# Kernel tuning notes

Hardware: AMD Instinct MI355X
Metric: run time of the kernel (lower is better)

Reference implementation:

```python
import jax, jax.numpy as jnp
import numpy as np

N, E, C, S = 30000, 480000, 256, 4
T_EVO = 0.1        # evolution_time
MAX_EIG = 0.5      # max_eigenval in create_ultra_stable_hamiltonian
MAX_NORM = 0.01    # max_norm in ultra_stable_matrix_exp
MAX_TERMS = 4
LN_EPS = 1e-5


def _build_subgraphs(edge_index, n, s):
    """Emulates the per-node k_hop=1 BFS (capped at max_subgraph_size=s) and the
    subgraph laplacian Hamiltonian build (edge_weight=0.1, self-loops added).
    Pure structural preprocessing: integer/constant w.r.t. all float params."""
    src = np.asarray(edge_index[0], dtype=np.int64)
    dst = np.asarray(edge_index[1], dtype=np.int64)
    loops = np.arange(n, dtype=np.int64)
    src = np.concatenate([src, loops]); dst = np.concatenate([dst, loops])
    order = np.argsort(src, kind='stable')
    src_s, dst_s = src[order], dst[order]
    starts = np.searchsorted(src_s, np.arange(n))
    ends = np.searchsorted(src_s, np.arange(n) + 1)
    edge_set = set((src * n + dst).tolist())
    sub_nodes = np.zeros((n, s), dtype=np.int64)
    sub_mask = np.zeros((n, s), dtype=np.float32)
    H = np.zeros((n, s, s), dtype=np.float32)
    for i in range(n):
        nbrs = [i]
        for d in dst_s[starts[i]:ends[i]]:
            d = int(d)
            if d != i and d not in nbrs:
                nbrs.append(d)
                if len(nbrs) == s:
                    break
        m = len(nbrs)
        sub_nodes[i, :m] = nbrs
        sub_nodes[i, m:] = i          # pad with center (masked out below)
        sub_mask[i, :m] = 1.0
        A = np.zeros((s, s), dtype=np.float32)
        for a in range(m):
            ka = nbrs[a] * n
            for b in range(m):
                if (ka + nbrs[b]) in edge_set:
                    A[a, b] = 1.0
        deg = np.maximum(A.sum(axis=1), 1e-6)   # degree(row), clamped like torch
        H[i] = np.diag(deg) - 0.1 * A           # laplacian with edge_weight=0.1
    return sub_nodes, sub_mask, H


def _mat_fro(M):
    return jnp.sqrt(jnp.sum(jnp.abs(M) ** 2, axis=(-2, -1)))


def _unitary_from_H(sub_H):
    """ultra_stable_matrix_exp, batched over N tiny [S,S] Hamiltonians.
    The torch .item() norm/eigenvalue rescales detach gradients, so treating this
    whole block as parameter-independent (it is: H is structural) is faithful."""
    Hc = sub_H.astype(jnp.complex64)
    ev = jnp.linalg.eigvals(Hc)                              # [N,S] (CPU op)
    mx = jnp.max(ev.real, axis=-1)
    Hc = Hc * jnp.where(mx > MAX_EIG, MAX_EIG / mx, 1.0)[:, None, None]
    hn = _mat_fro(Hc)
    Hc = Hc * jnp.where(hn > MAX_NORM, MAX_NORM / hn, 1.0)[:, None, None]
    A = (-1j) * Hc * (T_EVO * 0.1)                           # scaled_H
    I = jnp.eye(S, dtype=jnp.complex64)
    U = jnp.broadcast_to(I, Hc.shape)
    term = U
    for k in range(1, MAX_TERMS + 1):
        term = jnp.matmul(term, A) / k
        tn = _mat_fro(term)
        term = term * jnp.where(tn > 0.1, 0.1 / tn, 1.0)[:, None, None]
        U = U + term
    err = _mat_fro(jnp.matmul(U, jnp.conj(jnp.swapaxes(U, -1, -2))) - I)
    U = jnp.where((err > 0.1)[:, None, None], I + A * 0.01, U)
    return U


def _cplx_linear(xr, xi, wr, wi, br, bi):
    xr = jnp.clip(xr, -10.0, 10.0); xi = jnp.clip(xi, -10.0, 10.0)
    re = xr @ wr.T - xi @ wi.T + br
    im = xr @ wi.T + xi @ wr.T + bi
    return re + 1j * im


def _cln(z, w, b, eps=LN_EPS):
    # UltraStableComplexLayerNorm, training-mode batch stats over dim 0
    mag = jnp.clip(jnp.sqrt(z.real ** 2 + z.imag ** 2 + eps), eps, 1000.0)
    mean = mag.mean(0)
    var = mag.var(0)
    nm = (mag - mean) / (jnp.sqrt(var + eps) + eps)
    sm = jnp.clip(nm * jnp.abs(w) + b, eps, 10.0)
    ph = jnp.arctan2(jnp.clip(z.imag, -1e6, 1e6), jnp.clip(z.real, -1e6, 1e6) + 1e-10)
    return sm * jnp.cos(ph) + 1j * (sm * jnp.sin(ph))


def _crelu(z, leak=0.01, mx=5.0):
    r = jnp.clip(z.real, -mx, mx); i = jnp.clip(z.imag, -mx, mx)
    return jnp.where(r > 0, r, leak * r) + 1j * jnp.where(i > 0, i, leak * i)


def setup_inputs() -> dict:
    key = jax.random.key(0)
    k1, k2, k3, k4 = jax.random.split(key, 4)
    x = jax.random.normal(k1, (N, C), dtype=jnp.float32)
    edge_index = jax.random.randint(k2, (2, E), 0, N, dtype=jnp.int64)
    sub_nodes, sub_mask, sub_H = _build_subgraphs(np.asarray(edge_index), N, S)
    std = np.sqrt(0.5 / C).astype(np.float32)
    w_real = jax.random.normal(k3, (C, C), dtype=jnp.float32) * std
    w_imag = jax.random.normal(k4, (C, C), dtype=jnp.float32) * std
    return {
        'x': x,
        'edge_index': edge_index,
        'sub_nodes': jnp.asarray(sub_nodes),
        'sub_mask': jnp.asarray(sub_mask),
        'sub_H': jnp.asarray(sub_H),
        'w_real': w_real,
        'w_imag': w_imag,
        'b_real': jnp.zeros((C,), jnp.float32),
        'b_imag': jnp.zeros((C,), jnp.float32),
        'ln_weight': jnp.full((C,), 0.1, jnp.float32),
        'ln_bias': jnp.zeros((C,), jnp.float32),
        'evolution_scale': jnp.asarray(0.1, jnp.float32),
    }


def reference(x, edge_index, sub_nodes, sub_mask, sub_H,
              w_real, w_imag, b_real, b_imag, ln_weight, ln_bias,
              evolution_scale):
    # complex linear (input is real -> imag part zero, matching torch.complex(x, 0*x))
    h = _cplx_linear(x, jnp.zeros_like(x), w_real, w_imag, b_real, b_imag)  # [N,C] c64
    U = _unitary_from_H(sub_H)                                              # [N,S,S]
    sub_x = h[sub_nodes] * sub_mask[..., None]                              # [N,S,C]
    # center node is slot 0 of each subgraph -> take row 0 of U @ sub_x
    evolved = jnp.einsum('ns,nsc->nc', U[:, 0, :], sub_x)
    out = evolved * evolution_scale + x.astype(jnp.complex64)  # residual (in==out)
    out = _cln(out, ln_weight, ln_bias)
    out = _crelu(out)
    # dropout is eval-mode identity
    return jnp.concatenate([out.real, out.imag], axis=-1)      # [N, 2C] float32
```

## Files before the change

### kernel.cpp

```cpp
#include <hip/hip_runtime.h>
#include <stdint.h>

#define N_NODES 30000
#define NC 256

typedef _Float16 f16x8 __attribute__((ext_vector_type(8)));
typedef _Float16 f16x4 __attribute__((ext_vector_type(4)));
typedef _Float16 f16x2 __attribute__((ext_vector_type(2)));
typedef float f32x4 __attribute__((ext_vector_type(4)));

__global__ void k_conv_x(const float* __restrict__ x, _Float16* __restrict__ xb) {
    int i = (blockIdx.x * 256 + threadIdx.x) * 4;
    float4 v = *reinterpret_cast<const float4*>(x + i);
    f16x4 o;
    o[0] = (_Float16)fminf(fmaxf(v.x, -10.f), 10.f);
    o[1] = (_Float16)fminf(fmaxf(v.y, -10.f), 10.f);
    o[2] = (_Float16)fminf(fmaxf(v.z, -10.f), 10.f);
    o[3] = (_Float16)fminf(fmaxf(v.w, -10.f), 10.f);
    *reinterpret_cast<f16x4*>(xb + i) = o;
}

__global__ void k_conv_w(const float* __restrict__ wr, const float* __restrict__ wi,
                         _Float16* __restrict__ Wb) {
    int i = (blockIdx.x * 256 + threadIdx.x) * 4;
    const float* src = (i < NC * NC) ? (wr + i) : (wi + (i - NC * NC));
    float4 v = *reinterpret_cast<const float4*>(src);
    f16x4 o;
    o[0] = (_Float16)v.x; o[1] = (_Float16)v.y;
    o[2] = (_Float16)v.z; o[3] = (_Float16)v.w;
    *reinterpret_cast<f16x4*>(Wb + i) = o;
}

__global__ void k_prep(const float* __restrict__ subH, const float* __restrict__ sub_mask,
                       const float* __restrict__ escp, float* __restrict__ c4) {
    int node = blockIdx.x * 256 + threadIdx.x;
    if (node >= N_NODES) return;
    float esc = *escp;
    const float4* Hp = reinterpret_cast<const float4*>(subH + node * 16);
    float4 r0 = Hp[0], r1 = Hp[1], r2 = Hp[2], r3 = Hp[3];
    float fr = r0.x * r0.x + r0.y * r0.y + r0.z * r0.z + r0.w * r0.w
             + r1.x * r1.x + r1.y * r1.y + r1.z * r1.z + r1.w * r1.w
             + r2.x * r2.x + r2.y * r2.y + r2.z * r2.z + r2.w * r2.w
             + r3.x * r3.x + r3.y * r3.y + r3.z * r3.z + r3.w * r3.w;
    float coef = 1e-4f * rsqrtf(fr) * esc;
    float4 m = *reinterpret_cast<const float4*>(sub_mask + node * 4);
    float4 o;
    o.x = coef * r0.x * m.x;
    o.y = coef * r0.y * m.y;
    o.z = coef * r0.z * m.z;
    o.w = coef * r0.w * m.w;
    *reinterpret_cast<float4*>(c4 + node * 4) = o;
}

__global__ __launch_bounds__(256, 2) void k_gemm(
    const _Float16* __restrict__ A, const _Float16* __restrict__ B,
    const float* __restrict__ br, const float* __restrict__ bi,
    _Float16* __restrict__ H)
{
    int bid = blockIdx.x;
    int bm = bid >> 1, cs = bid & 1;
    int tid = threadIdx.x;
    int lane = tid & 63, wave = tid >> 6;
    int quad = lane >> 4, l16 = lane & 15;
    int wm = wave >> 1, wn = wave & 1;
    int row0 = bm * 128 + wm * 64;

    f16x8 af[4][8];
#pragma unroll
    for (int mi = 0; mi < 4; mi++) {
        int r = row0 + mi * 16 + l16;
        if (r >= N_NODES) r = N_NODES - 1;
        const _Float16* ap = A + r * NC + quad * 8;
#pragma unroll
        for (int kc = 0; kc < 8; kc++)
            af[mi][kc] = *reinterpret_cast<const f16x8*>(ap + kc * 32);
    }

    const float* bias_p = wn ? bi : br;
#pragma unroll
    for (int cn = 0; cn < 2; cn++) {
        const _Float16* bbase = B + ((wn ? 256 : 0) + cs * 128 + cn * 64 + l16) * NC
                                  + quad * 8;
        f16x8 bb[2][4];
#pragma unroll
        for (int ni = 0; ni < 4; ni++)
            bb[0][ni] = *reinterpret_cast<const f16x8*>(bbase + ni * 16 * NC);
        f32x4 acc[4][4] = {};
#pragma unroll
        for (int kc = 0; kc < 8; kc++) {
            int cur = kc & 1, nxt = cur ^ 1;
            if (kc < 7) {
#pragma unroll
                for (int ni = 0; ni < 4; ni++)
                    bb[nxt][ni] = *reinterpret_cast<const f16x8*>(
                        bbase + ni * 16 * NC + (kc + 1) * 32);
            }
#pragma unroll
            for (int mi = 0; mi < 4; mi++)
#pragma unroll
                for (int ni = 0; ni < 4; ni++)
                    acc[mi][ni] = __builtin_amdgcn_mfma_f32_16x16x32_f16(
                        af[mi][kc], bb[cur][ni], acc[mi][ni], 0, 0, 0);
        }
#pragma unroll
        for (int ni = 0; ni < 4; ni++) {
            int c = cs * 128 + cn * 64 + ni * 16 + l16;
            float bias = bias_p[c];
            int cc = 2 * c + wn;
#pragma unroll
            for (int mi = 0; mi < 4; mi++) {
                int rowb = row0 + mi * 16 + quad * 4;
#pragma unroll
                for (int r = 0; r < 4; r++) {
                    int row = rowb + r;
                    if (row < N_NODES)
                        H[row * 512 + cc] = (_Float16)(acc[mi][ni][r] + bias);
                }
            }
        }
    }
}

#define NPB 60
#define NGRP 8
__global__ __launch_bounds__(512) void k_evolve(
    const float* __restrict__ x, const int* __restrict__ sub_nodes,
    const float* __restrict__ c4, const _Float16* __restrict__ h,
    const float* __restrict__ escp,
    float* __restrict__ outz, _Float16* __restrict__ zbuf, int use_f16,
    float* __restrict__ ssum, float* __restrict__ ssumsq)
{
    __shared__ int   s_nodes[NPB][4];
    __shared__ float s_P[NPB][4];
    __shared__ float s_redA[NGRP][256];
    __shared__ float s_redB[NGRP][256];
    int tid = threadIdx.x;
    int g = tid >> 6, lane = tid & 63;
    int base = blockIdx.x * NPB;
    if (tid < NPB) {
        int node = base + tid;
        *reinterpret_cast<float4*>(&s_P[tid][0]) =
            *reinterpret_cast<const float4*>(c4 + node * 4);
        *reinterpret_cast<int4*>(&s_nodes[tid][0]) =
            *reinterpret_cast<const int4*>(sub_nodes + node * 4);
    }
    __syncthreads();
    float esc = *escp;
    float lsum[4] = {0.f, 0.f, 0.f, 0.f};
    float lsq[4]  = {0.f, 0.f, 0.f, 0.f};

    f16x8 hvA[4];
    float4 xA;
    int j = g;
#pragma unroll
    for (int s = 0; s < 4; s++)
        hvA[s] = *reinterpret_cast<const f16x8*>(h + s_nodes[j][s] * 512 + lane * 8);
    xA = *reinterpret_cast<const float4*>(x + (base + j) * NC + lane * 4);

    for (;;) {
        int jn = j + NGRP;
        bool more = jn < NPB;
        f16x8 hvB[4];
        float4 xB;
        if (more) {
#pragma unroll
            for (int s = 0; s < 4; s++)
                hvB[s] = *reinterpret_cast<const f16x8*>(
                    h + s_nodes[jn][s] * 512 + lane * 8);
            xB = *reinterpret_cast<const float4*>(x + (base + jn) * NC + lane * 4);
        }
        {
            int node = base + j;
            float P0 = s_P[j][0], P1 = s_P[j][1], P2 = s_P[j][2], P3 = s_P[j][3];
            float xr[4] = {xA.x, xA.y, xA.z, xA.w};
            f16x8 zo;
            float or4[4], oi4[4];
#pragma unroll
            for (int e = 0; e < 4; e++) {
                float hr0 = (float)hvA[0][2 * e], hi0 = (float)hvA[0][2 * e + 1];
                float hr1 = (float)hvA[1][2 * e], hi1 = (float)hvA[1][2 * e + 1];
                float hr2 = (float)hvA[2][2 * e], hi2 = (float)hvA[2][2 * e + 1];
                float hr3 = (float)hvA[3][2 * e], hi3 = (float)hvA[3][2 * e + 1];
                float er = esc * hr0;
                float ei = esc * hi0;
                er = fmaf(P0, hi0, er); ei = fmaf(-P0, hr0, ei);
                er = fmaf(P1, hi1, er); ei = fmaf(-P1, hr1, ei);
                er = fmaf(P2, hi2, er); ei = fmaf(-P2, hr2, ei);
                er = fmaf(P3, hi3, er); ei = fmaf(-P3, hr3, ei);
                float outr = er + xr[e];
                float outi = ei;
                or4[e] = outr; oi4[e] = outi;
                zo[2 * e] = (_Float16)outr; zo[2 * e + 1] = (_Float16)outi;
                float mag = sqrtf(fmaf(outr, outr, fmaf(outi, outi, 1e-5f)));
                mag = fminf(fmaxf(mag, 1e-5f), 1000.f);
                lsum[e] += mag;
                lsq[e] = fmaf(mag, mag, lsq[e]);
            }
            if (use_f16) {
                *reinterpret_cast<f16x8*>(zbuf + node * 512 + lane * 8) = zo;
            } else {
                *reinterpret_cast<float4*>(outz + node * 512 + lane * 4) =
                    make_float4(or4[0], or4[1], or4[2], or4[3]);
                *reinterpret_cast<float4*>(outz + node * 512 + 256 + lane * 4) =
                    make_float4(oi4[0], oi4[1], oi4[2], oi4[3]);
            }
        }
        if (!more) break;
#pragma unroll
        for (int s = 0; s < 4; s++) hvA[s] = hvB[s];
        xA = xB;
        j = jn;
    }
#pragma unroll
    for (int e = 0; e < 4; e++) {
        s_redA[g][lane * 4 + e] = lsum[e];
        s_redB[g][lane * 4 + e] = lsq[e];
    }
    __syncthreads();
    if (tid < 256) {
        float a = 0.f;
#pragma unroll
        for (int q = 0; q < NGRP; q++) a += s_redA[q][tid];
        atomicAdd(&ssum[tid], a);
    } else {
        int t = tid - 256;
        float b = 0.f;
#pragma unroll
        for (int q = 0; q < NGRP; q++) b += s_redB[q][t];
        atomicAdd(&ssumsq[t], b);
    }
}

__global__ __launch_bounds__(256) void k_norm(
    float* __restrict__ out, const _Float16* __restrict__ zbuf, int use_f16,
    const float* __restrict__ ssum, const float* __restrict__ ssumsq,
    const float* __restrict__ lnw, const float* __restrict__ lnb)
{
    int tid = threadIdx.x;
    int node = blockIdx.x * 4 + (tid >> 6);
    int c0 = (tid & 63) * 4;
    float re[4], im[4];
    if (use_f16) {
        f16x8 z = *reinterpret_cast<const f16x8*>(zbuf + node * 512 + c0 * 2);
#pragma unroll
        for (int e = 0; e < 4; e++) { re[e] = (float)z[2 * e]; im[e] = (float)z[2 * e + 1]; }
    } else {
        float4 r4 = *reinterpret_cast<const float4*>(out + node * 512 + c0);
        float4 i4 = *reinterpret_cast<const float4*>(out + node * 512 + 256 + c0);
        re[0] = r4.x; re[1] = r4.y; re[2] = r4.z; re[3] = r4.w;
        im[0] = i4.x; im[1] = i4.y; im[2] = i4.z; im[3] = i4.w;
    }
    float4 s4 = *reinterpret_cast<const float4*>(ssum + c0);
    float4 q4 = *reinterpret_cast<const float4*>(ssumsq + c0);
    float4 w4 = *reinterpret_cast<const float4*>(lnw + c0);
    float4 lb4 = *reinterpret_cast<const float4*>(lnb + c0);
    float S[4] = {s4.x, s4.y, s4.z, s4.w};
    float Q[4] = {q4.x, q4.y, q4.z, q4.w};
    float W[4] = {w4.x, w4.y, w4.z, w4.w};
    float L[4] = {lb4.x, lb4.y, lb4.z, lb4.w};
    const float invN = 1.0f / (float)N_NODES;
    float orr[4], oii[4];
#pragma unroll
    for (int e = 0; e < 4; e++) {
        float mean = S[e] * invN;
        float var = fmaxf(Q[e] * invN - mean * mean, 0.f);
        float denom = sqrtf(var + 1e-5f) + 1e-5f;
        float A = fabsf(W[e]) / denom;
        float Bc = L[e] - mean * A;
        float r = re[e], i = im[e];
        float mag = sqrtf(fmaf(r, r, fmaf(i, i, 1e-5f)));
        mag = fminf(fmaxf(mag, 1e-5f), 1000.f);
        float sm = fmaf(mag, A, Bc);
        sm = fminf(fmaxf(sm, 1e-5f), 10.0f);
        float px = fminf(fmaxf(r, -1e6f), 1e6f) + 1e-10f;
        float py = fminf(fmaxf(i, -1e6f), 1e6f);
        float r2 = fmaf(px, px, py * py);
        float inv = rsqrtf(r2);
        float zr = sm * px * inv, zi = sm * py * inv;
        zr = fminf(fmaxf(zr, -5.f), 5.f);
        zi = fminf(fmaxf(zi, -5.f), 5.f);
        orr[e] = zr > 0.f ? zr : 0.01f * zr;
        oii[e] = zi > 0.f ? zi : 0.01f * zi;
    }
    *reinterpret_cast<float4*>(out + node * 512 + c0) =
        make_float4(orr[0], orr[1], orr[2], orr[3]);
    *reinterpret_cast<float4*>(out + node * 512 + 256 + c0) =
        make_float4(oii[0], oii[1], oii[2], oii[3]);
}

extern "C" void kernel_launch(void* const* d_in, const int* in_sizes, int n_in,
                              void* d_out, int out_size, void* d_ws, size_t ws_size,
                              hipStream_t stream) {
    const float* x        = (const float*)d_in[0];
    const int*   sub_nodes = (const int*)d_in[2];
    const float* sub_mask  = (const float*)d_in[3];
    const float* subH      = (const float*)d_in[4];
    const float* wr  = (const float*)d_in[5];
    const float* wi  = (const float*)d_in[6];
    const float* br  = (const float*)d_in[7];
    const float* bi  = (const float*)d_in[8];
    const float* lnw = (const float*)d_in[9];
    const float* lnb = (const float*)d_in[10];
    const float* esc = (const float*)d_in[11];
    float* out = (float*)d_out;

    char* ws = (char*)d_ws;
    const size_t XB_OFF   = 0;
    const size_t WB_OFF   = 15360000;
    const size_t H_OFF    = 15622144;
    const size_t STAT_OFF = 46342144;
    const size_t C4_OFF   = 46346240;
    const size_t ZB_OFF   = 46826240;
    const size_t WS_NEED_F16 = ZB_OFF + 30720000;
    _Float16* xb = (_Float16*)(ws + XB_OFF);
    _Float16* Wb = (_Float16*)(ws + WB_OFF);
    _Float16* h  = (_Float16*)(ws + H_OFF);
    float* ssum   = (float*)(ws + STAT_OFF);
    float* ssumsq = (float*)(ws + STAT_OFF + 1024);
    float* c4     = (float*)(ws + C4_OFF);
    _Float16* zbuf = (_Float16*)(ws + ZB_OFF);
    int use_f16 = (ws_size >= WS_NEED_F16) ? 1 : 0;

    hipMemsetAsync(ssum, 0, 2048, stream);
    hipLaunchKernelGGL(k_conv_x, dim3(7500), dim3(256), 0, stream, x, xb);
    hipLaunchKernelGGL(k_conv_w, dim3(128), dim3(256), 0, stream, wr, wi, Wb);
    hipLaunchKernelGGL(k_prep, dim3(118), dim3(256), 0, stream,
                       subH, sub_mask, esc, c4);
    hipLaunchKernelGGL(k_gemm, dim3(235 * 2), dim3(256), 0, stream, xb, Wb, br, bi, h);
    hipLaunchKernelGGL(k_evolve, dim3(500), dim3(512), 0, stream,
                       x, sub_nodes, c4, h, esc, out, zbuf, use_f16,
                       ssum, ssumsq);
    hipLaunchKernelGGL(k_norm, dim3(7500), dim3(256), 0, stream,
                       out, zbuf, use_f16, ssum, ssumsq, lnw, lnb);
}
```

Measured before the change: 200.1 us.

## Shrink GEMM tiles to 64x64 per block for higher occupancy and more blocks

The complex-linear GEMM kernel moves from 128-row by 256-column blocks, which keep all A fragments in registers and double-buffer B, to 64-row by 64-column blocks that stream A and B from global memory each k-step. The grid grows from 470 to 1876 blocks and launch bounds allow 4 blocks per CU. The aim is to cut register pressure and fill the 256 CUs better. The cost is more redundant global/L2 reads of A and B and no explicit prefetch of the next k-step.

```diff
diff --git a/kernel.cpp b/kernel.cpp
--- a/kernel.cpp
+++ b/kernel.cpp
@@ -52,70 +52,60 @@
     *reinterpret_cast<float4*>(c4 + node * 4) = o;
 }
 
-__global__ __launch_bounds__(256, 2) void k_gemm(
+__global__ __launch_bounds__(256, 4) void k_gemm(
     const _Float16* __restrict__ A, const _Float16* __restrict__ B,
     const float* __restrict__ br, const float* __restrict__ bi,
     _Float16* __restrict__ H)
 {
     int bid = blockIdx.x;
-    int bm = bid >> 1, cs = bid & 1;
+    int bm = bid >> 2, cns = bid & 3;
     int tid = threadIdx.x;
     int lane = tid & 63, wave = tid >> 6;
     int quad = lane >> 4, l16 = lane & 15;
     int wm = wave >> 1, wn = wave & 1;
-    int row0 = bm * 128 + wm * 64;
-
-    f16x8 af[4][8];
-#pragma unroll
-    for (int mi = 0; mi < 4; mi++) {
-        int r = row0 + mi * 16 + l16;
-        if (r >= N_NODES) r = N_NODES - 1;
-        const _Float16* ap = A + r * NC + quad * 8;
-#pragma unroll
-        for (int kc = 0; kc < 8; kc++)
-            af[mi][kc] = *reinterpret_cast<const f16x8*>(ap + kc * 32);
-    }
+    int row0 = bm * 64 + wm * 32;
+
+    int r0 = row0 + l16;
+    int r1 = row0 + 16 + l16;
+    if (r0 >= N_NODES) r0 = N_NODES - 1;
+    if (r1 >= N_NODES) r1 = N_NODES - 1;
+    const _Float16* ap0 = A + r0 * NC + quad * 8;
+    const _Float16* ap1 = A + r1 * NC + quad * 8;
 
     const float* bias_p = wn ? bi : br;
-#pragma unroll
-    for (int cn = 0; cn < 2; cn++) {
-        const _Float16* bbase = B + ((wn ? 256 : 0) + cs * 128 + cn * 64 + l16) * NC
-                                  + quad * 8;
-        f16x8 bb[2][4];
-#pragma unroll
-        for (int ni = 0; ni < 4; ni++)
-            bb[0][ni] = *reinterpret_cast<const f16x8*>(bbase + ni * 16 * NC);
-        f32x4 acc[4][4] = {};
-#pragma unroll
-        for (int kc = 0; kc < 8; kc++) {
-            int cur = kc & 1, nxt = cur ^ 1;
-            if (kc < 7) {
-#pragma unroll
-                for (int ni = 0; ni < 4; ni++)
-                    bb[nxt][ni] = *reinterpret_cast<const f16x8*>(
-                        bbase + ni * 16 * NC + (kc + 1) * 32);
-            }
-#pragma unroll
-            for (int mi = 0; mi < 4; mi++)
-#pragma unroll
-                for (int ni = 0; ni < 4; ni++)
-                    acc[mi][ni] = __builtin_amdgcn_mfma_f32_16x16x32_f16(
-                        af[mi][kc], bb[cur][ni], acc[mi][ni], 0, 0, 0);
-        }
-#pragma unroll
-        for (int ni = 0; ni < 4; ni++) {
-            int c = cs * 128 + cn * 64 + ni * 16 + l16;
-            float bias = bias_p[c];
-            int cc = 2 * c + wn;
-#pragma unroll
-            for (int mi = 0; mi < 4; mi++) {
-                int rowb = row0 + mi * 16 + quad * 4;
-#pragma unroll
-                for (int r = 0; r < 4; r++) {
-                    int row = rowb + r;
-                    if (row < N_NODES)
-                        H[row * 512 + cc] = (_Float16)(acc[mi][ni][r] + bias);
-                }
+    const _Float16* bbase = B + ((wn ? 256 : 0) + cns * 64 + l16) * NC + quad * 8;
+
+    f32x4 acc[2][4] = {};
+#pragma unroll
+    for (int kc = 0; kc < 8; kc++) {
+        f16x8 a0 = *reinterpret_cast<const f16x8*>(ap0 + kc * 32);
+        f16x8 a1 = *reinterpret_cast<const f16x8*>(ap1 + kc * 32);
+        f16x8 b0 = *reinterpret_cast<const f16x8*>(bbase + 0 * 16 * NC + kc * 32);
+        f16x8 b1 = *reinterpret_cast<const f16x8*>(bbase + 1 * 16 * NC + kc * 32);
+        f16x8 b2 = *reinterpret_cast<const f16x8*>(bbase + 2 * 16 * NC + kc * 32);
+        f16x8 b3 = *reinterpret_cast<const f16x8*>(bbase + 3 * 16 * NC + kc * 32);
+        acc[0][0] = __builtin_amdgcn_mfma_f32_16x16x32_f16(a0, b0, acc[0][0], 0, 0, 0);
+        acc[0][1] = __builtin_amdgcn_mfma_f32_16x16x32_f16(a0, b1, acc[0][1], 0, 0, 0);
+        acc[0][2] = __builtin_amdgcn_mfma_f32_16x16x32_f16(a0, b2, acc[0][2], 0, 0, 0);
+        acc[0][3] = __builtin_amdgcn_mfma_f32_16x16x32_f16(a0, b3, acc[0][3], 0, 0, 0);
+        acc[1][0] = __builtin_amdgcn_mfma_f32_16x16x32_f16(a1, b0, acc[1][0], 0, 0, 0);
+        acc[1][1] = __builtin_amdgcn_mfma_f32_16x16x32_f16(a1, b1, acc[1][1], 0, 0, 0);
+        acc[1][2] = __builtin_amdgcn_mfma_f32_16x16x32_f16(a1, b2, acc[1][2], 0, 0, 0);
+        acc[1][3] = __builtin_amdgcn_mfma_f32_16x16x32_f16(a1, b3, acc[1][3], 0, 0, 0);
+    }
+#pragma unroll
+    for (int ni = 0; ni < 4; ni++) {
+        int c = cns * 64 + ni * 16 + l16;
+        float bias = bias_p[c];
+        int cc = 2 * c + wn;
+#pragma unroll
+        for (int mi = 0; mi < 2; mi++) {
+            int rowb = row0 + mi * 16 + quad * 4;
+#pragma unroll
+            for (int r = 0; r < 4; r++) {
+                int row = rowb + r;
+                if (row < N_NODES)
+                    H[row * 512 + cc] = (_Float16)(acc[mi][ni][r] + bias);
             }
         }
     }
@@ -326,7 +316,7 @@
     hipLaunchKernelGGL(k_conv_w, dim3(128), dim3(256), 0, stream, wr, wi, Wb);
     hipLaunchKernelGGL(k_prep, dim3(118), dim3(256), 0, stream,
                        subH, sub_mask, esc, c4);
-    hipLaunchKernelGGL(k_gemm, dim3(235 * 2), dim3(256), 0, stream, xb, Wb, br, bi, h);
+    hipLaunchKernelGGL(k_gemm, dim3(469 * 4), dim3(256), 0, stream, xb, Wb, br, bi, h);
     hipLaunchKernelGGL(k_evolve, dim3(500), dim3(512), 0, stream,
                        x, sub_nodes, c4, h, esc, out, zbuf, use_f16,
                        ssum, ssumsq);
```

Result: slower. 212.7 us (+6.3%).
